# Kernel tuning notes

Measured on AMD Instinct MI355X. Metric: run time of the kernel, lower is better.

The kernel has to match this reference:

```python
import jax, jax.numpy as jnp
import numpy as np

NUM_CLASSES = 14
IGNORE = 0
MAX_SAMPLES = 28 * 50
MAX_VIEWS = 50
TEMP = 0.1
THRESH = 0.3


def setup_inputs() -> dict:
    key = jax.random.key(0)
    B, Fd, D, H, W = 2, 128, 16, 128, 128
    N = B * D * H * W
    feats = jax.random.normal(key, (B, Fd, D, H, W), jnp.float32)
    idx = np.arange(N)
    pred = (idx % NUM_CLASSES).astype(np.int32)
    # alternate blocks: easy (label==pred) / hard (label!=pred) so every class
    # has >max_views pixels with >= n_view/2 hard and easy samples
    block = (idx // NUM_CLASSES) % 2
    lab = np.where(block == 0, pred, (pred + 1) % NUM_CLASSES).astype(np.int32)
    labels = jnp.asarray(lab.reshape(B, D, H, W))
    predict = jnp.asarray(pred.reshape(B, D, H, W))
    probability = jnp.ones((B, D, H, W), jnp.float32)
    queue = jax.random.normal(jax.random.fold_in(key, 1), (NUM_CLASSES, 4096, Fd), jnp.float32)
    return {"feats": feats, "labels": labels, "predict": predict,
            "probability": probability, "queue": queue}


def _l2n(x):
    return x / jnp.linalg.norm(x, axis=-1, keepdims=True)


def reference(feats, labels, predict, probability, queue):
    Fd = feats.shape[1]
    # [B, Fd, D, H, W] -> [N, Fd]
    f = jnp.transpose(feats, (0, 2, 3, 4, 1)).reshape(-1, Fd)
    lab = labels.reshape(-1)
    pred = predict.reshape(-1)
    valid = probability.reshape(-1) > THRESH
    N = f.shape[0]

    total_classes = NUM_CLASSES - 1              # all non-ignore classes qualify by construction
    n_view = min(MAX_SAMPLES // total_classes, MAX_VIEWS)  # = 50
    n_hard = n_view // 2                          # balanced branch always taken
    n_easy = n_view - n_hard
    idxs = jnp.arange(N)

    def pick(mask, k):
        # deterministic stand-in for randperm: first k valid indices
        keys = jnp.where(mask, idxs, N)
        return jnp.sort(keys)[:k]

    def sample_class(c):
        hard = valid & (pred == c) & (lab != c)
        easy = valid & (pred == c) & (lab == c)
        sel = jnp.concatenate([pick(hard, n_hard), pick(easy, n_easy)])
        return f[sel]

    classes = jnp.arange(1, NUM_CLASSES)
    X_ = jax.vmap(sample_class)(classes)          # [C-1, n_view, Fd]

    # positive queue: per-class mean of (threshold-filtered) feats
    onehot = jax.nn.one_hot(lab, NUM_CLASSES, dtype=f.dtype) * valid[:, None].astype(f.dtype)
    sums = jnp.einsum('nc,nd->cd', onehot, f)     # [C, Fd]
    cnts = onehot.sum(0)[:, None]
    pos_queue = sums / cnts                        # [C, Fd]

    # negatives: second half of cache, classes 1..C-1 (class 0 skipped in _sample_negative)
    neg = queue[1:, queue.shape[1] // 2:, :]       # [C-1, M, Fd]

    a = _l2n(X_)                                   # [C-1, V, Fd]
    p = _l2n(pos_queue[1:])                        # [C-1, Fd]
    n = _l2n(neg)                                  # [C-1, M, Fd]

    logits = jnp.einsum('cvd,cd->cv', a, p) / TEMP           # [C-1, V]
    neg_sum = jnp.exp(jnp.einsum('cvd,cmd->cvm', a, n) / TEMP).sum(-1)  # [C-1, V]
    log_prob = -logits + jnp.log(jnp.exp(logits) + neg_sum)
    # sum over classes of per-class mean, divided by num classes
    return log_prob.mean(axis=1).mean()
```

## Files before the change

### kernel.cpp

```cpp
#include <hip/hip_runtime.h>

#define NUMC 14
#define FD 128
#define SPATIAL (16*128*128)
#define N_TOTAL (2*SPATIAL)
#define NV 50
#define NH 25
#define TC 13
#define QLEN 4096
#define MCH 64
#define NCHUNK 32
#define NSTR (FD + 4)
#define NNEGBLK (TC * NCHUNK)
#define THRESH_F 0.3f

#define RSTR 17
#define PXB 32768
#define CHB (SPATIAL / PXB)
#define NSUMBLK (256 * CHB)
#define NPI 64

typedef float f32x4 __attribute__((ext_vector_type(4)));

#define WS_SEL     0
#define WS_LOSSP   656
#define WS_CNT0    672
#define WS_NEGPART 680
#define WS_ANORM   21480
#define WS_AROWS   22144
#define WS_PART    105344
#define WS_LAB8    220032

__global__ __launch_bounds__(256) void k_pre(const int* __restrict__ labels,
        const int* __restrict__ predict, const float* __restrict__ prob,
        unsigned char* __restrict__ lab8, int* __restrict__ sel, int* __restrict__ cnt0) {
    int blk = blockIdx.x;
    int tid = threadIdx.x;
    if (blk < 512) {
        int n = blk * 1024 + tid * 4;
        int4   lb = *(const int4*)(labels + n);
        float4 pv = *(const float4*)(prob + n);
        uchar4 o;
        o.x = pv.x > THRESH_F ? (unsigned char)(lb.x & 15) : (unsigned char)15;
        o.y = pv.y > THRESH_F ? (unsigned char)(lb.y & 15) : (unsigned char)15;
        o.z = pv.z > THRESH_F ? (unsigned char)(lb.z & 15) : (unsigned char)15;
        o.w = pv.w > THRESH_F ? (unsigned char)(lb.w & 15) : (unsigned char)15;
        *(uchar4*)(lab8 + n) = o;
    } else if (blk < 538) {
        __shared__ unsigned long long masks[4];
        int cat = blk - 512;
        int c = 1 + (cat >> 1);
        bool hard = (cat & 1) == 0;
        int lane = tid & 63, w = tid >> 6;
        int* slot = sel + (c - 1) * NV + (hard ? 0 : NH);
        int found = 0;
        for (int base = 0; base < N_TOTAL && found < NH; base += 256) {
            int n = base + tid;
            int pr = predict[n];
            int lb = labels[n];
            float pb = prob[n];
            bool m = (pr == c) && (pb > THRESH_F) && (hard ? (lb != c) : (lb == c));
            unsigned long long mk = __ballot(m);
            if (lane == 0) masks[w] = mk;
            __syncthreads();
            int pre = 0;
            #pragma unroll
            for (int j = 0; j < 4; ++j) {
                unsigned long long mj = masks[j];
                if (j < w) pre += __popcll(mj);
            }
            int rank = found + pre + __popcll(mk & ((1ull << lane) - 1ull));
            if (m && rank < NH) slot[rank] = n;
            found += __popcll(masks[0]) + __popcll(masks[1])
                   + __popcll(masks[2]) + __popcll(masks[3]);
            __syncthreads();
        }
        if (tid < NH && tid >= found) slot[tid] = N_TOTAL - 1;
    } else {
        if (tid == 0) cnt0[0] = 0;
    }
}

__global__ __launch_bounds__(128) void k_gather(const float* __restrict__ feats,
        const int* __restrict__ sel, float* __restrict__ arows, float* __restrict__ anorm) {
    __shared__ float red[2];
    int r = blockIdx.x;
    int t = threadIdx.x;
    int n = sel[r];
    int b = n >> 18, sp = n & (SPATIAL - 1);
    float v = feats[((size_t)(b * FD + t)) * SPATIAL + sp];
    arows[r * FD + t] = v;
    float a = v * v;
    #pragma unroll
    for (int o = 32; o; o >>= 1) a += __shfl_xor(a, o);
    if ((t & 63) == 0) red[t >> 6] = a;
    __syncthreads();
    if (t == 0) anorm[r] = sqrtf(red[0] + red[1]);
}

__global__ __launch_bounds__(256) void k_neg(const float* __restrict__ queue,
        const float* __restrict__ arows, const float* __restrict__ anorm,
        float* __restrict__ negpart) {
    __shared__ float n_s[MCH * NSTR];
    __shared__ float an_s[NV];
    int tid = threadIdx.x;
    int lane = tid & 63, w = tid >> 6;
    int ci = blockIdx.x >> 5;
    int chunk = blockIdx.x & 31;
    if (tid < NV) an_s[tid] = anorm[ci * NV + tid];
    const float* qp = queue + ((size_t)(ci + 1) * QLEN + (QLEN / 2) + chunk * MCH) * (size_t)FD;
    for (int i = tid; i < MCH * (FD / 4); i += 256) {
        int m = i >> 5, k4 = i & 31;
        ((float4*)(n_s + m * NSTR))[k4] = ((const float4*)qp)[i];
    }
    __syncthreads();
    const float4* nrow = (const float4*)(n_s + lane * NSTR);
    float sq = 0.f;
    #pragma unroll
    for (int k = 0; k < FD / 4; ++k) {
        float4 t = nrow[k];
        sq += t.x*t.x + t.y*t.y + t.z*t.z + t.w*t.w;
    }
    float inn = 10.f * rsqrtf(sq);
    float* np = negpart + (size_t)(ci * NV) * NCHUNK + chunk;
    const float4* abase = (const float4*)(arows + (size_t)(ci * NV) * FD);
    for (int v = w; v < NV; v += 4) {
        const float4* a4 = abase + v * (FD / 4);
        float dot = 0.f;
        #pragma unroll
        for (int k = 0; k < FD / 4; ++k) {
            float4 x = a4[k], y = nrow[k];
            dot += x.x*y.x + x.y*y.y + x.z*y.z + x.w*y.w;
        }
        float e = __expf(dot * inn / an_s[v]);
        #pragma unroll
        for (int o = 32; o; o >>= 1) e += __shfl_xor(e, o);
        if (lane == 0) np[(size_t)v * NCHUNK] = e;
    }
}

__global__ __launch_bounds__(256) void k_sums(const float* __restrict__ feats,
        const unsigned char* __restrict__ lab8, float* __restrict__ part) {
    __shared__ float smem[256 * RSTR];
    int tid = threadIdx.x;
    int plane = blockIdx.x >> 3;
    int chunk = blockIdx.x & (CHB - 1);
    int b = plane >> 7;
    int ch = plane & 127;
    int r0 = tid * RSTR;
    #pragma unroll
    for (int k = 0; k < RSTR; ++k) smem[r0 + k] = 0.f;

    const f32x4*  fp4 = (const f32x4*)(feats + (size_t)plane * SPATIAL) + (chunk << 13);
    const uchar4* lp4 = (const uchar4*)(lab8 + (size_t)b * SPATIAL) + (chunk << 13);
    f32x4  v = fp4[tid];
    uchar4 u = lp4[tid];
    for (int i = 0; i < 31; ++i) {
        f32x4  vn = fp4[(i + 1) * 256 + tid];
        uchar4 un = lp4[(i + 1) * 256 + tid];
        smem[r0 + (u.x & 15)] += v.x;
        smem[r0 + (u.y & 15)] += v.y;
        smem[r0 + (u.z & 15)] += v.z;
        smem[r0 + (u.w & 15)] += v.w;
        v = vn; u = un;
    }
    smem[r0 + (u.x & 15)] += v.x;
    smem[r0 + (u.y & 15)] += v.y;
    smem[r0 + (u.z & 15)] += v.z;
    smem[r0 + (u.w & 15)] += v.w;

    int lane = tid & 63, w = tid >> 6;
    int pi = b * 32 + chunk * 4 + w;
    #pragma unroll
    for (int c = 0; c < NUMC; ++c) {
        float x = smem[r0 + c];
        #pragma unroll
        for (int o = 32; o; o >>= 1) x += __shfl_xor(x, o);
        if (lane == 0) part[((size_t)c * FD + ch) * NPI + pi] = x;
    }
}

__global__ __launch_bounds__(256) void k_loss(const float* __restrict__ arows,
        const float* __restrict__ anorm, const float* __restrict__ part,
        const float* __restrict__ negpart, float* __restrict__ lossp,
        int* __restrict__ cnt0, float* __restrict__ out) {
    __shared__ float p_s[FD];
    __shared__ float red_s[2];
    __shared__ float lacc[8];
    int tid = threadIdx.x;
    int ci = blockIdx.x, c = ci + 1;
    if (tid < 128) {
        const float* pp = part + ((size_t)c * FD + tid) * NPI;
        float s = 0.f;
        #pragma unroll 8
        for (int k = 0; k < NPI; ++k) s += pp[k];
        p_s[tid] = s;
    }
    __syncthreads();
    if (tid < 128) {
        float q = p_s[tid] * p_s[tid];
        #pragma unroll
        for (int o = 32; o; o >>= 1) q += __shfl_xor(q, o);
        if ((tid & 63) == 0) red_s[tid >> 6] = q;
    }
    __syncthreads();
    float pninv10 = 10.f * rsqrtf(red_s[0] + red_s[1]);
    int grp = tid >> 5, l32 = tid & 31;
    float acc = 0.f;
    for (int r = grp; r < NV; r += 8) {
        int ar = ci * NV + r;
        const float4* a4 = (const float4*)(arows + (size_t)ar * FD);
        const float4* p4 = (const float4*)p_s;
        float4 x = a4[l32], y = p4[l32];
        float d = x.x*y.x + x.y*y.y + x.z*y.z + x.w*y.w;
        float ns = negpart[(size_t)ar * NCHUNK + l32];
        #pragma unroll
        for (int o = 16; o; o >>= 1) { d += __shfl_xor(d, o); ns += __shfl_xor(ns, o); }
        if (l32 == 0) {
            float logit = d * pninv10 / anorm[ar];
            acc += -logit + logf(__expf(logit) + ns);
        }
    }
    if (l32 == 0) lacc[grp] = acc;
    __syncthreads();
    if (tid == 0) {
        float s = 0.f;
        #pragma unroll
        for (int i = 0; i < 8; ++i) s += lacc[i];
        lossp[ci] = s;
        __threadfence();
        int t = atomicAdd(cnt0, 1);
        if (t == TC - 1) {
            __threadfence();
            float tot = 0.f;
            for (int i = 0; i < TC; ++i)
                tot += __hip_atomic_load(lossp + i, __ATOMIC_RELAXED, __HIP_MEMORY_SCOPE_AGENT);
            out[0] = tot * (1.f / (TC * NV));
        }
    }
}

extern "C" void kernel_launch(void* const* d_in, const int* in_sizes, int n_in,
                              void* d_out, int out_size, void* d_ws, size_t ws_size,
                              hipStream_t stream) {
    (void)in_sizes; (void)n_in; (void)out_size; (void)ws_size;
    const float* feats   = (const float*)d_in[0];
    const int*   labels  = (const int*)d_in[1];
    const int*   predict = (const int*)d_in[2];
    const float* prob    = (const float*)d_in[3];
    const float* queue   = (const float*)d_in[4];
    float* ws  = (float*)d_ws;
    float* out = (float*)d_out;

    int*   sel     = (int*)(ws + WS_SEL);
    float* lossp   = ws + WS_LOSSP;
    int*   cnt0    = (int*)(ws + WS_CNT0);
    float* negpart = ws + WS_NEGPART;
    float* anorm   = ws + WS_ANORM;
    float* arows   = ws + WS_AROWS;
    float* part    = ws + WS_PART;
    unsigned char* lab8 = (unsigned char*)(ws + WS_LAB8);

    k_pre    <<<539, 256, 0, stream>>>(labels, predict, prob, lab8, sel, cnt0);
    k_gather <<<TC * NV, 128, 0, stream>>>(feats, sel, arows, anorm);
    k_neg    <<<NNEGBLK, 256, 0, stream>>>(queue, arows, anorm, negpart);
    k_sums   <<<NSUMBLK, 256, 0, stream>>>(feats, lab8, part);
    k_loss   <<<TC, 256, 0, stream>>>(arows, anorm, part, negpart, lossp, cnt0, out);
}
```

Before: 100.3 us.

## Merge negative-logit and class-sum kernels into one heterogeneous launch

```diff
diff --git a/kernel.cpp b/kernel.cpp
--- a/kernel.cpp
+++ b/kernel.cpp
@@ -8,8 +8,8 @@
 #define NH 25
 #define TC 13
 #define QLEN 4096
-#define MCH 64
-#define NCHUNK 32
+#define MCH 32
+#define NCHUNK 64
 #define NSTR (FD + 4)
 #define NNEGBLK (TC * NCHUNK)
 #define THRESH_F 0.3f
@@ -26,10 +26,10 @@
 #define WS_LOSSP   656
 #define WS_CNT0    672
 #define WS_NEGPART 680
-#define WS_ANORM   21480
-#define WS_AROWS   22144
-#define WS_PART    105344
-#define WS_LAB8    220032
+#define WS_ANORM   42280
+#define WS_AROWS   42944
+#define WS_PART    126144
+#define WS_LAB8    240832
 
 __global__ __launch_bounds__(256) void k_pre(const int* __restrict__ labels,
         const int* __restrict__ predict, const float* __restrict__ prob,
@@ -98,85 +98,87 @@
     if (t == 0) anorm[r] = sqrtf(red[0] + red[1]);
 }
 
-__global__ __launch_bounds__(256) void k_neg(const float* __restrict__ queue,
+__global__ __launch_bounds__(256, 8) void k_main(const float* __restrict__ feats,
+        const unsigned char* __restrict__ lab8, const float* __restrict__ queue,
         const float* __restrict__ arows, const float* __restrict__ anorm,
-        float* __restrict__ negpart) {
-    __shared__ float n_s[MCH * NSTR];
-    __shared__ float an_s[NV];
+        float* __restrict__ part, float* __restrict__ negpart) {
+    __shared__ float smem[256 * RSTR];
     int tid = threadIdx.x;
     int lane = tid & 63, w = tid >> 6;
-    int ci = blockIdx.x >> 5;
-    int chunk = blockIdx.x & 31;
-    if (tid < NV) an_s[tid] = anorm[ci * NV + tid];
-    const float* qp = queue + ((size_t)(ci + 1) * QLEN + (QLEN / 2) + chunk * MCH) * (size_t)FD;
-    for (int i = tid; i < MCH * (FD / 4); i += 256) {
-        int m = i >> 5, k4 = i & 31;
-        ((float4*)(n_s + m * NSTR))[k4] = ((const float4*)qp)[i];
-    }
-    __syncthreads();
-    const float4* nrow = (const float4*)(n_s + lane * NSTR);
-    float sq = 0.f;
-    #pragma unroll
-    for (int k = 0; k < FD / 4; ++k) {
-        float4 t = nrow[k];
-        sq += t.x*t.x + t.y*t.y + t.z*t.z + t.w*t.w;
-    }
-    float inn = 10.f * rsqrtf(sq);
-    float* np = negpart + (size_t)(ci * NV) * NCHUNK + chunk;
-    const float4* abase = (const float4*)(arows + (size_t)(ci * NV) * FD);
-    for (int v = w; v < NV; v += 4) {
-        const float4* a4 = abase + v * (FD / 4);
-        float dot = 0.f;
+
+    if (blockIdx.x < NNEGBLK) {
+        int ci = blockIdx.x >> 6;
+        int chunk = blockIdx.x & 63;
+        float* n_s  = smem;
+        float* an_s = smem + 4224;
+        if (tid < NV) an_s[tid] = anorm[ci * NV + tid];
+        const float4* qp4 = (const float4*)(queue
+            + ((size_t)(ci + 1) * QLEN + (QLEN / 2) + chunk * MCH) * (size_t)FD);
+        for (int i = tid; i < MCH * (FD / 4); i += 256) {
+            int m = i >> 5, k4 = i & 31;
+            ((float4*)(n_s + m * NSTR))[k4] = qp4[i];
+        }
+        __syncthreads();
+        int half = lane >> 5, l32 = lane & 31;
+        const float4* nrow = (const float4*)(n_s + l32 * NSTR);
+        float sq = 0.f;
         #pragma unroll
         for (int k = 0; k < FD / 4; ++k) {
-            float4 x = a4[k], y = nrow[k];
-            dot += x.x*y.x + x.y*y.y + x.z*y.z + x.w*y.w;
-        }
-        float e = __expf(dot * inn / an_s[v]);
-        #pragma unroll
-        for (int o = 32; o; o >>= 1) e += __shfl_xor(e, o);
-        if (lane == 0) np[(size_t)v * NCHUNK] = e;
-    }
-}
-
-__global__ __launch_bounds__(256) void k_sums(const float* __restrict__ feats,
-        const unsigned char* __restrict__ lab8, float* __restrict__ part) {
-    __shared__ float smem[256 * RSTR];
-    int tid = threadIdx.x;
-    int plane = blockIdx.x >> 3;
-    int chunk = blockIdx.x & (CHB - 1);
-    int b = plane >> 7;
-    int ch = plane & 127;
-    int r0 = tid * RSTR;
-    #pragma unroll
-    for (int k = 0; k < RSTR; ++k) smem[r0 + k] = 0.f;
-
-    const f32x4*  fp4 = (const f32x4*)(feats + (size_t)plane * SPATIAL) + (chunk << 13);
-    const uchar4* lp4 = (const uchar4*)(lab8 + (size_t)b * SPATIAL) + (chunk << 13);
-    f32x4  v = fp4[tid];
-    uchar4 u = lp4[tid];
-    for (int i = 0; i < 31; ++i) {
-        f32x4  vn = fp4[(i + 1) * 256 + tid];
-        uchar4 un = lp4[(i + 1) * 256 + tid];
+            float4 t = nrow[k];
+            sq += t.x*t.x + t.y*t.y + t.z*t.z + t.w*t.w;
+        }
+        float inn = 10.f * rsqrtf(sq);
+        float* np = negpart + (size_t)(ci * NV) * NCHUNK + chunk;
+        const float4* abase = (const float4*)(arows + (size_t)(ci * NV) * FD);
+        for (int v = w * 2 + half; v < NV; v += 8) {
+            const float4* a4 = abase + v * (FD / 4);
+            float dot = 0.f;
+            #pragma unroll
+            for (int k = 0; k < FD / 4; ++k) {
+                float4 x = a4[k], y = nrow[k];
+                dot += x.x*y.x + x.y*y.y + x.z*y.z + x.w*y.w;
+            }
+            float e = __expf(dot * inn / an_s[v]);
+            #pragma unroll
+            for (int o = 16; o; o >>= 1) e += __shfl_xor(e, o);
+            if (l32 == 0) np[(size_t)v * NCHUNK] = e;
+        }
+    } else {
+        int sb = blockIdx.x - NNEGBLK;
+        int plane = sb >> 3;
+        int chunk = sb & (CHB - 1);
+        int b = plane >> 7;
+        int ch = plane & 127;
+        int r0 = tid * RSTR;
+        #pragma unroll
+        for (int k = 0; k < RSTR; ++k) smem[r0 + k] = 0.f;
+
+        const f32x4*  fp4 = (const f32x4*)(feats + (size_t)plane * SPATIAL) + (chunk << 13);
+        const uchar4* lp4 = (const uchar4*)(lab8 + (size_t)b * SPATIAL) + (chunk << 13);
+        f32x4  v = fp4[tid];
+        uchar4 u = lp4[tid];
+        for (int i = 0; i < 31; ++i) {
+            f32x4  vn = fp4[(i + 1) * 256 + tid];
+            uchar4 un = lp4[(i + 1) * 256 + tid];
+            smem[r0 + (u.x & 15)] += v.x;
+            smem[r0 + (u.y & 15)] += v.y;
+            smem[r0 + (u.z & 15)] += v.z;
+            smem[r0 + (u.w & 15)] += v.w;
+            v = vn; u = un;
+        }
         smem[r0 + (u.x & 15)] += v.x;
         smem[r0 + (u.y & 15)] += v.y;
         smem[r0 + (u.z & 15)] += v.z;
         smem[r0 + (u.w & 15)] += v.w;
-        v = vn; u = un;
-    }
-    smem[r0 + (u.x & 15)] += v.x;
-    smem[r0 + (u.y & 15)] += v.y;
-    smem[r0 + (u.z & 15)] += v.z;
-    smem[r0 + (u.w & 15)] += v.w;
-
-    int lane = tid & 63, w = tid >> 6;
-    int pi = b * 32 + chunk * 4 + w;
-    #pragma unroll
-    for (int c = 0; c < NUMC; ++c) {
-        float x = smem[r0 + c];
-        #pragma unroll
-        for (int o = 32; o; o >>= 1) x += __shfl_xor(x, o);
-        if (lane == 0) part[((size_t)c * FD + ch) * NPI + pi] = x;
+
+        int pi = b * 32 + chunk * 4 + w;
+        #pragma unroll
+        for (int c = 0; c < NUMC; ++c) {
+            float x = smem[r0 + c];
+            #pragma unroll
+            for (int o = 32; o; o >>= 1) x += __shfl_xor(x, o);
+            if (lane == 0) part[((size_t)c * FD + ch) * NPI + pi] = x;
+        }
     }
 }
 
@@ -213,7 +215,8 @@
         const float4* p4 = (const float4*)p_s;
         float4 x = a4[l32], y = p4[l32];
         float d = x.x*y.x + x.y*y.y + x.z*y.z + x.w*y.w;
-        float ns = negpart[(size_t)ar * NCHUNK + l32];
+        float ns = negpart[(size_t)ar * NCHUNK + l32]
+                 + negpart[(size_t)ar * NCHUNK + 32 + l32];
         #pragma unroll
         for (int o = 16; o; o >>= 1) { d += __shfl_xor(d, o); ns += __shfl_xor(ns, o); }
         if (l32 == 0) {
@@ -263,7 +266,6 @@
 
     k_pre    <<<539, 256, 0, stream>>>(labels, predict, prob, lab8, sel, cnt0);
     k_gather <<<TC * NV, 128, 0, stream>>>(feats, sel, arows, anorm);
-    k_neg    <<<NNEGBLK, 256, 0, stream>>>(queue, arows, anorm, negpart);
-    k_sums   <<<NSUMBLK, 256, 0, stream>>>(feats, lab8, part);
+    k_main   <<<NNEGBLK + NSUMBLK, 256, 0, stream>>>(feats, lab8, queue, arows, anorm, part, negpart);
     k_loss   <<<TC, 256, 0, stream>>>(arows, anorm, part, negpart, lossp, cnt0, out);
 }
```

Measured after the change: 175.5 us. 1.75x slower.
